# Kernel optimization log

Measured on AMD Instinct MI355X. Metric: run time of the kernel, lower is better.

The kernel has to match this reference:

```python
import jax, jax.numpy as jnp
import numpy as np

# dims chosen per input_specs / init_kwargs
B, S, D_IN, UNITS, WIN = 4, 2048, 512, 64, 32
W = 2 * WIN + 1  # max window length


def setup_inputs() -> dict:
    key = jax.random.key(0)
    ks = jax.random.split(key, 8)
    p = lambda k, shape: jax.random.normal(k, shape, dtype=jnp.float32) * 0.02
    return {
        "query": jax.random.normal(ks[0], (B, S, D_IN), dtype=jnp.float32),
        "value": jax.random.normal(ks[1], (B, S, D_IN), dtype=jnp.float32),
        "Wq": p(ks[2], (D_IN, UNITS)), "bq": jnp.zeros((UNITS,), jnp.float32),
        "Wk": p(ks[3], (D_IN, UNITS)), "bk": jnp.zeros((UNITS,), jnp.float32),
        "Wv": p(ks[4], (D_IN, UNITS)), "bv": jnp.zeros((UNITS,), jnp.float32),
    }


def reference(query, value, Wq, bq, Wk, bk, Wv, bv):
    # Dense projections (query stream -> Q, value stream -> K and V)
    Q = query @ Wq + bq
    K = value @ Wk + bk
    V = value @ Wv + bv

    i = np.arange(S)
    start = np.maximum(i - WIN, 0)            # [S]
    end = np.minimum(i + WIN + 1, S)          # [S]
    lengths = end - start                      # [S] window length per position
    offsets = np.concatenate([[0], np.cumsum(lengths)[:-1]])
    L = int(lengths.sum())                     # total output seq length (concat of all windows)

    idx = start[:, None] + np.arange(W)[None, :]   # [S, W] window token indices
    valid = idx < end[:, None]                      # [S, W] which slots exist
    idx_c = np.minimum(idx, S - 1)                  # clamp for safe gather

    idx_c = jnp.asarray(idx_c)
    valid_j = jnp.asarray(valid)

    # Gather overlapping windows: [B, S, W, UNITS]
    Ql = Q[:, idx_c]
    Kl = K[:, idx_c]
    Vl = V[:, idx_c]

    # Faithful to original: ALL window rows act as queries for window i.
    scale = 1.0 / jnp.sqrt(jnp.asarray(UNITS, dtype=Q.dtype))
    scores = jnp.einsum("bswd,bsud->bswu", Ql, Kl) * scale  # [B, S, W, W]
    neg = jnp.finfo(scores.dtype).min
    scores = jnp.where(valid_j[None, :, None, :], scores, neg)  # mask padded keys
    weights = jax.nn.softmax(scores, axis=-1)
    out_local = jnp.einsum("bswu,bsud->bswd", weights, Vl)  # [B, S, W, UNITS]

    # Concat valid rows of every window along seq axis -> [B, L, UNITS]
    flat_pos = jnp.asarray(offsets)[:, None] + jnp.arange(W)[None, :]  # [S, W]
    flat_pos = jnp.where(valid_j, flat_pos, L)  # invalid rows dumped in slot L
    out = jnp.zeros((Q.shape[0], L + 1, UNITS), dtype=out_local.dtype)
    out = out.at[:, flat_pos.reshape(-1)].set(out_local.reshape(Q.shape[0], -1, UNITS))
    return out[:, :L]
```

## Files before the change

kernel.cpp:

```cpp
#include <hip/hip_runtime.h>
#include <hip/hip_bf16.h>

#define BB 4
#define SS 2048
#define DIN 512
#define UU 64
#define WINR 32
#define LTOT 132064
#define GQ 16
#define VST 200

typedef __attribute__((ext_vector_type(8))) short short8;
typedef __attribute__((ext_vector_type(4))) float float4v;
typedef __attribute__((ext_vector_type(4))) uint uint4v;

static __device__ __forceinline__ ushort f2bf(float f) {
    union { __hip_bfloat16 h; ushort u; } c;
    c.h = __float2bfloat16(f);
    return c.u;
}
static __device__ __forceinline__ float bf2f(ushort u) {
    union { float f; uint v; } c;
    c.v = ((uint)u) << 16;
    return c.f;
}
static __device__ __forceinline__ float bfbits(uint u) {
    union { float f; uint v; } c;
    c.v = u;
    return c.f;
}

__device__ __forceinline__ int offs_of(int s) {
    int a = s < (SS - 33) ? s : (SS - 33);
    int m = (s - 33) > 0 ? (s - 33) : 0;
    return a * (a - 1) / 2 + 33 * a + (s - a) * SS - m * (m + 1) / 2;
}

__global__ __launch_bounds__(256) void prep_w(
    const float* __restrict__ Wq, const float* __restrict__ Wk, const float* __restrict__ Wv,
    ushort* __restrict__ Wt)
{
    __shared__ float T[64][65];
    const int mtx = blockIdx.x >> 3;
    const int kc  = blockIdx.x & 7;
    const float* W = (mtx == 0) ? Wq : ((mtx == 1) ? Wk : Wv);
    const int tid = threadIdx.x;
    for (int idx = tid; idx < 64 * 64; idx += 256) {
        const int k = idx >> 6, n = idx & 63;
        T[n][k] = W[(size_t)(kc * 64 + k) * UU + n];
    }
    __syncthreads();
    for (int idx = tid; idx < 64 * 64; idx += 256) {
        const int n = idx >> 6, kl = idx & 63;
        Wt[(size_t)mtx * UU * DIN + (size_t)n * DIN + kc * 64 + kl] = f2bf(T[n][kl]);
    }
}

__global__ __launch_bounds__(256) void qkv_mfma(
    const float* __restrict__ query, const float* __restrict__ value,
    const ushort* __restrict__ Wt,
    const float* __restrict__ bq, const float* __restrict__ bk, const float* __restrict__ bv,
    float* __restrict__ Qs, ushort* __restrict__ Kf, ushort* __restrict__ Vf)
{
    __shared__ float red[4][16 * UU];
    const int bid = blockIdx.x;
    const int mtx = bid >> 9;
    const int rt  = bid & 511;
    const int tid = threadIdx.x;
    const int kq = tid >> 6;
    const int lane = tid & 63;
    const int m16 = lane & 15, quad = lane >> 4;

    const float* X = (mtx == 0) ? query : value;
    const float* Xrow = X + (size_t)(rt * 16 + m16) * DIN + kq * 128 + quad * 8;
    const ushort* Wm = Wt + (size_t)mtx * UU * DIN + (size_t)m16 * DIN + kq * 128 + quad * 8;

    float4v acc[4];
#pragma unroll
    for (int nb = 0; nb < 4; ++nb) acc[nb] = (float4v){0.f, 0.f, 0.f, 0.f};

#pragma unroll
    for (int kk = 0; kk < 4; ++kk) {
        const float4 xa = *(const float4*)(Xrow + kk * 32);
        const float4 xb = *(const float4*)(Xrow + kk * 32 + 4);
        short8 a;
        a[0] = (short)f2bf(xa.x); a[1] = (short)f2bf(xa.y);
        a[2] = (short)f2bf(xa.z); a[3] = (short)f2bf(xa.w);
        a[4] = (short)f2bf(xb.x); a[5] = (short)f2bf(xb.y);
        a[6] = (short)f2bf(xb.z); a[7] = (short)f2bf(xb.w);
#pragma unroll
        for (int nb = 0; nb < 4; ++nb) {
            const short8 bfr = *(const short8*)(Wm + (size_t)nb * 16 * DIN + kk * 32);
            acc[nb] = __builtin_amdgcn_mfma_f32_16x16x32_bf16(a, bfr, acc[nb], 0, 0, 0);
        }
    }

#pragma unroll
    for (int nb = 0; nb < 4; ++nb)
#pragma unroll
        for (int reg = 0; reg < 4; ++reg)
            red[kq][(quad * 4 + reg) * UU + nb * 16 + m16] = acc[nb][reg];
    __syncthreads();

    const float* bias = (mtx == 0) ? bq : ((mtx == 1) ? bk : bv);
#pragma unroll
    for (int i = 0; i < 4; ++i) {
        const int e = tid + 256 * i;
        const int col = e & 63, row = e >> 6;
        float s = red[0][e] + red[1][e] + red[2][e] + red[3][e] + bias[col];
        const size_t gi = (size_t)(rt * 16 + row) * UU + col;
        if (mtx == 0)      Qs[gi] = s * 0.125f;
        else if (mtx == 1) Kf[gi] = f2bf(s);
        else               Vf[gi] = f2bf(s);
    }
}

__global__ __launch_bounds__(1024) void attn_kernel(
    const float* __restrict__ Qs, const ushort* __restrict__ Kf,
    const ushort* __restrict__ Vf, float* __restrict__ out)
{
    __shared__ ushort Vt[UU * VST];
    __shared__ float  evf[GQ * VST];

    const int blk = blockIdx.x;
    const int b = blk >> 7;
    const int q0 = (blk & 127) << 4;
    const int tid = threadIdx.x;
    const int lane = tid & 63;
    const int wq = __builtin_amdgcn_readfirstlane(tid >> 6);

    const int j0 = max(q0 - 2 * WINR, 0);
    const int j1 = min(q0 + GQ - 1 + 2 * WINR + 1, SS);
    const int nw = j1 - j0;

    for (int idx = tid; idx < UU * VST / 2; idx += 1024) ((uint*)Vt)[idx] = 0u;
    if (tid < GQ * 40) evf[(tid / 40) * VST + (tid % 40)] = 0.f;
    __syncthreads();

    const uint* Vg = (const uint*)(Vf + ((size_t)b * SS + j0) * UU);
    for (int idx = tid; idx < nw * 32; idx += 1024) {
        const int j = idx >> 5, d2 = idx & 31;
        const uint v = Vg[idx];
        Vt[(2 * d2) * VST + 40 + j]     = (ushort)v;
        Vt[(2 * d2 + 1) * VST + 40 + j] = (ushort)(v >> 16);
    }
    __syncthreads();

    const int qi = q0 + wq;
    const int blo = max(qi - 2 * WINR, 0);
    const int bhi = min(qi + 2 * WINR + 1, SS);
    const float* qp = Qs + ((size_t)b * SS + qi) * UU;
#pragma unroll
    for (int pass = 0; pass < 3; ++pass) {
        const int jj = pass * 64 + lane;
        const int j = j0 + jj;
        const bool live = (jj < nw) && (j >= blo) && (j < bhi);
        const uint* kr = (const uint*)(Kf + ((size_t)b * SS + (live ? j : j0)) * UU);
        float dot = 0.f;
#pragma unroll
        for (int c = 0; c < 8; ++c) {
            const uint4v kp = *(const uint4v*)(kr + c * 4);
#pragma unroll
            for (int u = 0; u < 4; ++u) {
                dot = fmaf(qp[c * 8 + 2 * u],     bfbits(kp[u] << 16),         dot);
                dot = fmaf(qp[c * 8 + 2 * u + 1], bfbits(kp[u] & 0xffff0000u), dot);
            }
        }
        const float e = live ? __expf(dot) : 0.f;
        if (jj < VST - 40) evf[wq * VST + 40 + jj] = e;
    }
    __syncthreads();

    const int s_lo = max(qi - WINR, 0);
    const int s_hi = min(qi + WINR, SS - 1);
    const int a = (s_lo - j0 - 7) & 7;
    const int s_start = s_lo - a;
    const int I_s = s_start - j0 + 8;
    const int I_f = I_s - 7;
    const int A0 = I_f + 72;

    const ushort* vrow = Vt + lane * VST;
    const float*  erow = evf + wq * VST;

    float accA = 0.f, denA = 0.f, accR = 0.f, denR = 0.f;
#pragma unroll
    for (int t = 0; t < 9; ++t) {
        const int base = I_f + 8 * t;
        const uint4v  vv = *(const uint4v*)(vrow + base);
        const float4v e0 = *(const float4v*)(erow + base);
        const float4v e1 = *(const float4v*)(erow + base + 4);
#pragma unroll
        for (int k = 0; k < 8; ++k) {
            const float e = (k < 4) ? e0[k] : e1[k - 4];
            const uint wv = vv[k >> 1];
            const float v = (k & 1) ? bfbits(wv & 0xffff0000u) : bfbits(wv << 16);
            accA = fmaf(e, v, accA);
            denA += e;
        }
    }

    float pE7 = erow[I_s];
    float pV7 = bf2f(vrow[I_s]);

    int off = offs_of(s_lo);
    float* outb = out + (size_t)b * LTOT * UU;
    const int ng = (s_hi - s_start + 8) >> 3;
    for (int g = 0; g < ng; ++g) {
        const int Ab = A0 + 8 * g;
        const uint4v  Av  = *(const uint4v*)(vrow + Ab);
        const float4v Ae0 = *(const float4v*)(erow + Ab);
        const float4v Ae1 = *(const float4v*)(erow + Ab + 4);
        const int Rb = I_f + 8 * (g + 1);
        const uint4v  Rv  = *(const uint4v*)(vrow + Rb);
        const float4v Re0 = *(const float4v*)(erow + Rb);
        const float4v Re1 = *(const float4v*)(erow + Rb + 4);
        int s = s_start + 8 * g;
#pragma unroll
        for (int k = 0; k < 8; ++k, ++s) {
            if (s >= s_lo && s <= s_hi) {
                const int st = (s - WINR > 0) ? s - WINR : 0;
                const int en = (s + WINR + 1 < SS) ? s + WINR + 1 : SS;
                const float r = __builtin_amdgcn_rcpf(denA - denR);
                outb[(size_t)(off + qi - st) * UU + lane] = (accA - accR) * r;
                off += en - st;
            }
            {
                const float e = (k < 4) ? Ae0[k] : Ae1[k - 4];
                const uint wv = Av[k >> 1];
                const float v = (k & 1) ? bfbits(wv & 0xffff0000u) : bfbits(wv << 16);
                accA = fmaf(e, v, accA);
                denA += e;
            }
            {
                float e, v;
                if (k == 0) { e = pE7; v = pV7; }
                else {
                    const int m = k - 1;
                    e = (m < 4) ? Re0[m] : Re1[m - 4];
                    const uint wv = Rv[m >> 1];
                    v = (m & 1) ? bfbits(wv & 0xffff0000u) : bfbits(wv << 16);
                }
                accR = fmaf(e, v, accR);
                denR += e;
            }
        }
        pE7 = Re1[3];
        pV7 = bfbits(Rv[3] & 0xffff0000u);
    }
}

extern "C" void kernel_launch(void* const* d_in, const int* in_sizes, int n_in,
                              void* d_out, int out_size, void* d_ws, size_t ws_size,
                              hipStream_t stream) {
    const float* query = (const float*)d_in[0];
    const float* value = (const float*)d_in[1];
    const float* Wq = (const float*)d_in[2];
    const float* bq = (const float*)d_in[3];
    const float* Wk = (const float*)d_in[4];
    const float* bk = (const float*)d_in[5];
    const float* Wv = (const float*)d_in[6];
    const float* bv = (const float*)d_in[7];
    float* out = (float*)d_out;

    float* Qs = (float*)d_ws;
    ushort* Kf = (ushort*)(Qs + (size_t)BB * SS * UU);
    ushort* Vf = Kf + (size_t)BB * SS * UU;
    ushort* Wt = (ushort*)((float*)d_out + (size_t)out_size) - (size_t)3 * UU * DIN;

    prep_w<<<24, 256, 0, stream>>>(Wq, Wk, Wv, Wt);
    qkv_mfma<<<3 * 512, 256, 0, stream>>>(query, value, Wt, bq, bk, bv, Qs, Kf, Vf);
    attn_kernel<<<512, 1024, 0, stream>>>(Qs, Kf, Vf, out);
}
```

Measured before the change: 215.4 us.

## Compute attention scores with bf16 MFMA and overlap with V staging

The per-lane scalar FMA dot products for query-key scores are replaced by MFMA 16x16x32 bf16 instructions. Q is split into hi and lo bf16 parts so precision stays close to fp32. Nine waves compute the score tile while the other seven waves transpose V into shared memory at the same time, which removes one barrier phase. Shared-memory zeroing is vectorised, and the launch bounds now request 8 waves per EU. This adds some MFMA rounding error and relies on the window masking being reproduced correctly.

```diff
diff --git a/kernel.cpp b/kernel.cpp
--- a/kernel.cpp
+++ b/kernel.cpp
@@ -115,12 +115,12 @@
     }
 }
 
-__global__ __launch_bounds__(1024) void attn_kernel(
+__global__ __launch_bounds__(1024, 8) void attn_kernel(
     const float* __restrict__ Qs, const ushort* __restrict__ Kf,
     const ushort* __restrict__ Vf, float* __restrict__ out)
 {
-    __shared__ ushort Vt[UU * VST];
-    __shared__ float  evf[GQ * VST];
+    __shared__ __align__(16) ushort Vt[UU * VST];
+    __shared__ __align__(16) float  evf[GQ * VST];
 
     const int blk = blockIdx.x;
     const int b = blk >> 7;
@@ -133,44 +133,57 @@
     const int j1 = min(q0 + GQ - 1 + 2 * WINR + 1, SS);
     const int nw = j1 - j0;
 
-    for (int idx = tid; idx < UU * VST / 2; idx += 1024) ((uint*)Vt)[idx] = 0u;
-    if (tid < GQ * 40) evf[(tid / 40) * VST + (tid % 40)] = 0.f;
-    __syncthreads();
-
-    const uint* Vg = (const uint*)(Vf + ((size_t)b * SS + j0) * UU);
-    for (int idx = tid; idx < nw * 32; idx += 1024) {
-        const int j = idx >> 5, d2 = idx & 31;
-        const uint v = Vg[idx];
-        Vt[(2 * d2) * VST + 40 + j]     = (ushort)v;
-        Vt[(2 * d2 + 1) * VST + 40 + j] = (ushort)(v >> 16);
+    {
+        const uint4v z = (uint4v){0u, 0u, 0u, 0u};
+        uint4v* V4 = (uint4v*)Vt;
+        uint4v* E4 = (uint4v*)evf;
+        for (int i = tid; i < 1600; i += 1024) V4[i] = z;
+        for (int i = tid; i < 800;  i += 1024) E4[i] = z;
+    }
+    __syncthreads();
+
+    if (wq >= 9) {
+        const uint* Vg = (const uint*)(Vf + ((size_t)b * SS + j0) * UU);
+        for (int idx = tid - 9 * 64; idx < nw * 32; idx += 7 * 64) {
+            const int j = idx >> 5, d2 = idx & 31;
+            const uint v = Vg[idx];
+            Vt[(2 * d2) * VST + 40 + j]     = (ushort)v;
+            Vt[(2 * d2 + 1) * VST + 40 + j] = (ushort)(v >> 16);
+        }
+    } else {
+        const int t = wq;
+        const int m16 = lane & 15, quad = lane >> 4;
+        const int jb = j0 + 16 * t + m16;
+        const int jr = jb < SS ? jb : SS - 1;
+        const ushort* kr = Kf + ((size_t)b * SS + jr) * UU + quad * 8;
+        const float*  qr = Qs + ((size_t)b * SS + q0 + m16) * UU + quad * 8;
+        const short8 kb0 = *(const short8*)(kr);
+        const short8 kb1 = *(const short8*)(kr + 32);
+        short8 ah0, al0, ah1, al1;
+#pragma unroll
+        for (int e = 0; e < 8; ++e) {
+            const float qa = qr[e], qb = qr[e + 32];
+            const ushort h0 = f2bf(qa);
+            ah0[e] = (short)h0; al0[e] = (short)f2bf(qa - bf2f(h0));
+            const ushort h1 = f2bf(qb);
+            ah1[e] = (short)h1; al1[e] = (short)f2bf(qb - bf2f(h1));
+        }
+        float4v acc = (float4v){0.f, 0.f, 0.f, 0.f};
+        acc = __builtin_amdgcn_mfma_f32_16x16x32_bf16(ah0, kb0, acc, 0, 0, 0);
+        acc = __builtin_amdgcn_mfma_f32_16x16x32_bf16(al0, kb0, acc, 0, 0, 0);
+        acc = __builtin_amdgcn_mfma_f32_16x16x32_bf16(ah1, kb1, acc, 0, 0, 0);
+        acc = __builtin_amdgcn_mfma_f32_16x16x32_bf16(al1, kb1, acc, 0, 0, 0);
+#pragma unroll
+        for (int r = 0; r < 4; ++r) {
+            const int m = quad * 4 + r;
+            const int d = jb - (q0 + m);
+            const bool in = (d >= -64) && (d <= 64) && (jb < SS);
+            evf[m * VST + 40 + 16 * t + m16] = in ? __expf(acc[r]) : 0.f;
+        }
     }
     __syncthreads();
 
     const int qi = q0 + wq;
-    const int blo = max(qi - 2 * WINR, 0);
-    const int bhi = min(qi + 2 * WINR + 1, SS);
-    const float* qp = Qs + ((size_t)b * SS + qi) * UU;
-#pragma unroll
-    for (int pass = 0; pass < 3; ++pass) {
-        const int jj = pass * 64 + lane;
-        const int j = j0 + jj;
-        const bool live = (jj < nw) && (j >= blo) && (j < bhi);
-        const uint* kr = (const uint*)(Kf + ((size_t)b * SS + (live ? j : j0)) * UU);
-        float dot = 0.f;
-#pragma unroll
-        for (int c = 0; c < 8; ++c) {
-            const uint4v kp = *(const uint4v*)(kr + c * 4);
-#pragma unroll
-            for (int u = 0; u < 4; ++u) {
-                dot = fmaf(qp[c * 8 + 2 * u],     bfbits(kp[u] << 16),         dot);
-                dot = fmaf(qp[c * 8 + 2 * u + 1], bfbits(kp[u] & 0xffff0000u), dot);
-            }
-        }
-        const float e = live ? __expf(dot) : 0.f;
-        if (jj < VST - 40) evf[wq * VST + 40 + jj] = e;
-    }
-    __syncthreads();
-
     const int s_lo = max(qi - WINR, 0);
     const int s_hi = min(qi + WINR, SS - 1);
     const int a = (s_lo - j0 - 7) & 7;
```

New measurement: 198.6 us. 7.8% less time.
